# Kernel optimization log

Hardware: AMD Instinct MI355X
Metric: run time of the kernel (lower is better)

The kernel has to match this reference:

```python
import jax, jax.numpy as jnp
import numpy as np

B = 64            # number of graphs in the batch
D = 128           # in_node_dim
NUM_VIEWS = 4
MAX_NODES = 508   # max(node_counts) for the deterministic counts below


def _make_counts():
    # deterministic ragged node counts: 256, 260, ..., 508
    return jnp.asarray(256 + 4 * np.arange(B), dtype=jnp.int64)


def setup_inputs() -> dict:
    key = jax.random.key(0)
    node_counts = _make_counts()
    total = int(np.sum(256 + 4 * np.arange(B)))  # 24448
    z_nodes = jax.random.normal(key, (total, D), dtype=jnp.float32)
    return {"z_nodes": z_nodes, "node_counts": node_counts}


def reference(z_nodes, node_counts):
    # Pad ragged node embeddings into a dense [B, MAX_NODES, D] block with
    # zero rows for padding; then padded z @ z^T directly equals the
    # zero-padded per-graph adjacency logits (outer products with zero rows
    # are zero), matching the torch loop + torch.zeros pad.
    offsets = jnp.concatenate([jnp.zeros((1,), node_counts.dtype),
                               jnp.cumsum(node_counts)[:-1]])          # [B]
    pos = jnp.arange(MAX_NODES)                                        # [M]
    valid = pos[None, :] < node_counts[:, None]                        # [B, M]
    idx = jnp.where(valid, offsets[:, None] + pos[None, :], 0)         # [B, M]
    z_pad = z_nodes[idx] * valid[..., None].astype(z_nodes.dtype)      # [B, M, D]
    adj = jnp.einsum('bnd,bmd->bnm', z_pad, z_pad)                     # [B, M, M]
    # unsqueeze(1).repeat(1, V, 1, 1)
    return jnp.broadcast_to(adj[:, None], (B, NUM_VIEWS, MAX_NODES, MAX_NODES))
```

## Files before the change

### kernel.cpp

```cpp
#include <hip/hip_runtime.h>
#include <stdint.h>


typedef __bf16          v8bf __attribute__((ext_vector_type(8)));
typedef unsigned short  v8us __attribute__((ext_vector_type(8)));
typedef float           v4f  __attribute__((ext_vector_type(4)));
typedef unsigned int    v4u  __attribute__((ext_vector_type(4)));

#define NMAX  508
#define DD    128
#define NV    4
#define TOTAL 24448
#define IMG   (NMAX * NMAX)
#define IMGV4 (IMG / 4)
#define ROWV4 (NMAX / 4)
#define LDS2  516

__device__ __forceinline__ unsigned short f32_to_bf16_rne(float f) {
    unsigned int u = __builtin_bit_cast(unsigned int, f);
    u = (u + 0x7fffu + ((u >> 16) & 1u)) >> 16;
    return (unsigned short)u;
}

__device__ __forceinline__ v8us pack8(v4f lo, v4f hi) {
    v8us u;
    u[0] = f32_to_bf16_rne(lo.x); u[1] = f32_to_bf16_rne(lo.y);
    u[2] = f32_to_bf16_rne(lo.z); u[3] = f32_to_bf16_rne(lo.w);
    u[4] = f32_to_bf16_rne(hi.x); u[5] = f32_to_bf16_rne(hi.y);
    u[6] = f32_to_bf16_rne(hi.z); u[7] = f32_to_bf16_rne(hi.w);
    return u;
}

__global__ __launch_bounds__(256)
void cvt_transpose_kernel(const float* __restrict__ z,
                          unsigned short* __restrict__ zt)
{
    const int r   = blockIdx.x * 256 + threadIdx.x;
    const int koi = blockIdx.y;
    if (r >= TOTAL) return;
    const float* p = z + (size_t)r * DD + koi * 8;
    const v4f lo = *(const v4f*)p;
    const v4f hi = *(const v4f*)(p + 4);
    *(v8us*)(zt + ((size_t)koi * TOTAL + r) * 8) = pack8(lo, hi);
}

__global__ __launch_bounds__(256, 4)
void adj_gram_zt_kernel(const unsigned short* __restrict__ zt,
                        const int* __restrict__ counts,
                        float* __restrict__ out)
{
    __shared__ __align__(16) float sC[16 * LDS2];

    const int blk  = blockIdx.x;
    const int wgid = (blk & 7) * 256 + (blk >> 3);
    const int b    = wgid >> 5;
    const int i0   = (wgid & 31) * 16;

    const int tid  = threadIdx.x;
    const int lane = tid & 63;
    const int wave = tid >> 6;
    const int j0   = wave * 128;

    const bool is64 = (counts[1] == 0);
    int cnt = is64 ? counts[2 * lane] : counts[lane];
    int inc = cnt;
    #pragma unroll
    for (int s = 1; s < 64; s <<= 1) {
        int t = __shfl_up(inc, s);
        if (lane >= s) inc += t;
    }
    const int n   = __shfl(cnt, b);
    const int off = __shfl(inc, b) - n;

    const int lr = lane & 15;
    const int lg = lane >> 4;

    v4f acc[8];
    #pragma unroll
    for (int nt = 0; nt < 8; ++nt) acc[nt] = (v4f)0.0f;

    if (i0 < n) {
        #pragma unroll
        for (int ks = 0; ks < 4; ++ks) {
            const int koi = ks * 4 + lg;
            const unsigned short* pl = zt + (size_t)koi * TOTAL * 8;
            v8bf af, bfv[8];
            {
                const int r = i0 + lr;
                af = (r < n) ? *(const v8bf*)(pl + (size_t)(off + r) * 8)
                             : (v8bf)(__bf16)0.0f;
            }
            #pragma unroll
            for (int nt = 0; nt < 8; ++nt) {
                const int r = j0 + nt * 16 + lr;
                bfv[nt] = (r < n) ? *(const v8bf*)(pl + (size_t)(off + r) * 8)
                                  : (v8bf)(__bf16)0.0f;
            }
            #pragma unroll
            for (int nt = 0; nt < 8; ++nt)
                acc[nt] = __builtin_amdgcn_mfma_f32_16x16x32_bf16(
                    af, bfv[nt], acc[nt], 0, 0, 0);
        }
    }

    const int crow = lg * 4;
    #pragma unroll
    for (int nt = 0; nt < 8; ++nt)
        #pragma unroll
        for (int rr = 0; rr < 4; ++rr)
            sC[(crow + rr) * LDS2 + j0 + nt * 16 + lr] = acc[nt][rr];
    __syncthreads();

    const int rowsv = (NMAX - i0 < 16) ? (NMAX - i0) : 16;
    const int nvec  = rowsv * ROWV4;
    const size_t base = (size_t)(b * NV) * IMGV4 + (size_t)i0 * ROWV4;
    #pragma unroll
    for (int grp = 0; grp < 2; ++grp) {
        const size_t G0g = base + (size_t)grp * IMGV4;
        const size_t Gag = G0g & ~(size_t)7;
        const size_t G1g = G0g + (size_t)nvec;
        #pragma unroll
        for (int it = 0; it < 8; ++it) {
            const size_t g = Gag + tid + (size_t)it * 256;
            if (g >= G0g && g < G1g) {
                const int f   = (int)(g - G0g);
                const int row = f / ROWV4;
                const int c4  = f - row * ROWV4;
                const v4u val = *(const v4u*)&sC[row * LDS2 + c4 * 4];
                *(v4u*)(out + g * 4) = val;
                *(v4u*)(out + (g + 2 * (size_t)IMGV4) * 4) = val;
            }
        }
    }
}

__global__ __launch_bounds__(256, 4)
void adj_gram_fb_kernel(const float* __restrict__ z,
                        const int*   __restrict__ counts,
                        float*       __restrict__ out)
{
    __shared__ __align__(16) float sC[16 * LDS2];
    const int blk = blockIdx.x;
    const int b   = blk >> 5;
    const int i0  = (blk & 31) * 16;
    const int tid  = threadIdx.x;
    const int lane = tid & 63;
    const int wave = tid >> 6;
    const int j0   = wave * 128;
    const bool is64 = (counts[1] == 0);
    int cnt = is64 ? counts[2 * lane] : counts[lane];
    int inc = cnt;
    #pragma unroll
    for (int s = 1; s < 64; s <<= 1) {
        int t = __shfl_up(inc, s);
        if (lane >= s) inc += t;
    }
    const int n   = __shfl(cnt, b);
    const int off = __shfl(inc, b) - n;
    const int lr = lane & 15;
    const int lk = (lane >> 4) * 8;
    v4f acc[8];
    #pragma unroll
    for (int nt = 0; nt < 8; ++nt) acc[nt] = (v4f)0.0f;
    if (i0 < n) {
        const float* zb = z + (size_t)off * DD;
        #pragma unroll
        for (int ks = 0; ks < 4; ++ks) {
            const int ko = ks * 32 + lk;
            v8bf af, bfv[8];
            {
                const int r = i0 + lr;
                v4f lo = (v4f)0.0f, hi = (v4f)0.0f;
                if (r < n) {
                    const float* p = zb + (size_t)r * DD + ko;
                    lo = *(const v4f*)p; hi = *(const v4f*)(p + 4);
                }
                af = __builtin_bit_cast(v8bf, pack8(lo, hi));
            }
            #pragma unroll
            for (int nt = 0; nt < 8; ++nt) {
                const int r = j0 + nt * 16 + lr;
                v4f lo = (v4f)0.0f, hi = (v4f)0.0f;
                if (r < n) {
                    const float* p = zb + (size_t)r * DD + ko;
                    lo = *(const v4f*)p; hi = *(const v4f*)(p + 4);
                }
                bfv[nt] = __builtin_bit_cast(v8bf, pack8(lo, hi));
            }
            #pragma unroll
            for (int nt = 0; nt < 8; ++nt)
                acc[nt] = __builtin_amdgcn_mfma_f32_16x16x32_bf16(
                    af, bfv[nt], acc[nt], 0, 0, 0);
        }
    }
    const int crow = (lane >> 4) * 4;
    #pragma unroll
    for (int nt = 0; nt < 8; ++nt)
        #pragma unroll
        for (int rr = 0; rr < 4; ++rr)
            sC[(crow + rr) * LDS2 + j0 + nt * 16 + lr] = acc[nt][rr];
    __syncthreads();
    const int rowsv = (NMAX - i0 < 16) ? (NMAX - i0) : 16;
    const int nvec  = rowsv * ROWV4;
    for (int v = 0; v < NV; ++v) {
        const size_t G0 = (size_t)(b * NV + v) * IMGV4 + (size_t)i0 * ROWV4;
        const size_t Ga = G0 & ~(size_t)7;
        const size_t G1 = G0 + (size_t)nvec;
        for (size_t g = Ga + tid; g < G1; g += 256) {
            if (g < G0) continue;
            const int f   = (int)(g - G0);
            const int row = f / ROWV4;
            const int c4  = f - row * ROWV4;
            *(v4u*)(out + g * 4) = *(const v4u*)&sC[row * LDS2 + c4 * 4];
        }
    }
}

extern "C" void kernel_launch(void* const* d_in, const int* in_sizes, int n_in,
                              void* d_out, int out_size, void* d_ws, size_t ws_size,
                              hipStream_t stream) {
    const float* z      = (const float*)d_in[0];
    const int*   counts = (const int*)d_in[1];
    float*       out    = (float*)d_out;
    const size_t need   = (size_t)TOTAL * 16 * 16;

    if (d_ws != nullptr && ws_size >= need) {
        unsigned short* zt = (unsigned short*)d_ws;
        cvt_transpose_kernel<<<dim3((TOTAL + 255) / 256, 16), dim3(256), 0, stream>>>(
            z, zt);
        adj_gram_zt_kernel<<<dim3(64 * 32), dim3(256), 0, stream>>>(zt, counts, out);
    } else {
        adj_gram_fb_kernel<<<dim3(64 * 32), dim3(256), 0, stream>>>(z, counts, out);
    }
}
```

Baseline: 269.0 us.

## Write only view 0 in gram kernel, replicate other views in separate copy kernel

The gram kernel now stores only the first view of each graph's adjacency, where it previously stored two views per store group. A new kernel then reads view 0 back from global memory and writes views 1-3. This lightens the compute kernel's store epilogue, but it adds an extra kernel launch and an extra global read of view 0 (about 66 MB) on top of the same total writes. The copy also reads data that may no longer be in cache.

```diff
diff --git a/kernel.cpp b/kernel.cpp
--- a/kernel.cpp
+++ b/kernel.cpp
@@ -45,7 +45,7 @@
 }
 
 __global__ __launch_bounds__(256, 4)
-void adj_gram_zt_kernel(const unsigned short* __restrict__ zt,
+void adj_gram_v0_kernel(const unsigned short* __restrict__ zt,
                         const int* __restrict__ counts,
                         float* __restrict__ out)
 {
@@ -113,24 +113,31 @@
 
     const int rowsv = (NMAX - i0 < 16) ? (NMAX - i0) : 16;
     const int nvec  = rowsv * ROWV4;
-    const size_t base = (size_t)(b * NV) * IMGV4 + (size_t)i0 * ROWV4;
-    #pragma unroll
-    for (int grp = 0; grp < 2; ++grp) {
-        const size_t G0g = base + (size_t)grp * IMGV4;
-        const size_t Gag = G0g & ~(size_t)7;
-        const size_t G1g = G0g + (size_t)nvec;
-        #pragma unroll
-        for (int it = 0; it < 8; ++it) {
-            const size_t g = Gag + tid + (size_t)it * 256;
-            if (g >= G0g && g < G1g) {
-                const int f   = (int)(g - G0g);
-                const int row = f / ROWV4;
-                const int c4  = f - row * ROWV4;
-                const v4u val = *(const v4u*)&sC[row * LDS2 + c4 * 4];
-                *(v4u*)(out + g * 4) = val;
-                *(v4u*)(out + (g + 2 * (size_t)IMGV4) * 4) = val;
-            }
-        }
+    const size_t G0 = (size_t)(b * NV) * IMGV4 + (size_t)i0 * ROWV4;
+    #pragma unroll
+    for (int it = 0; it < 8; ++it) {
+        const int f = tid + it * 256;
+        if (f < nvec) {
+            const int row = f / ROWV4;
+            const int c4  = f - row * ROWV4;
+            *(v4u*)(out + (G0 + (size_t)f) * 4) = *(const v4u*)&sC[row * LDS2 + c4 * 4];
+        }
+    }
+}
+
+__global__ __launch_bounds__(256)
+void replicate_views_kernel(float* __restrict__ out)
+{
+    const int y = blockIdx.y;
+    const int b = y / 3;
+    const int v = 1 + y - b * 3;
+    const size_t base0 = (size_t)(b * NV) * IMGV4;
+    const size_t G0    = base0 + (size_t)v * IMGV4;
+    const size_t Ga    = G0 & ~(size_t)7;
+    const size_t g     = Ga + (size_t)blockIdx.x * 256 + threadIdx.x;
+    if (g >= G0 && g < G0 + (size_t)IMGV4) {
+        const v4u val = *(const v4u*)(out + (g - (size_t)v * IMGV4) * 4);
+        *(v4u*)(out + g * 4) = val;
     }
 }
 
@@ -228,7 +235,8 @@
         unsigned short* zt = (unsigned short*)d_ws;
         cvt_transpose_kernel<<<dim3((TOTAL + 255) / 256, 16), dim3(256), 0, stream>>>(
             z, zt);
-        adj_gram_zt_kernel<<<dim3(64 * 32), dim3(256), 0, stream>>>(zt, counts, out);
+        adj_gram_v0_kernel<<<dim3(64 * 32), dim3(256), 0, stream>>>(zt, counts, out);
+        replicate_views_kernel<<<dim3(253, 192), dim3(256), 0, stream>>>(out);
     } else {
         adj_gram_fb_kernel<<<dim3(64 * 32), dim3(256), 0, stream>>>(z, counts, out);
     }
```

After: 293.4 us. +9.0%, slower.
